# Kernel tuning notes

Measured on AMD Instinct MI355X. Metric: run time of the kernel, lower is better.

Reference implementation:

```python
import jax, jax.numpy as jnp
import numpy as np

LN_EPS = 1e-5

def setup_inputs() -> dict:
    key = jax.random.key(0)
    k1, k2, k3, k4 = jax.random.split(key, 4)
    B, N, F, O = 8, 2048, 256, 256
    x = jax.random.normal(k1, (B, N, F), dtype=jnp.float32)
    adj = jax.random.uniform(k2, (B, N, N), dtype=jnp.float32)
    # LayerNorm affine params
    gamma = jnp.ones((F,), jnp.float32)
    beta = jnp.zeros((F,), jnp.float32)
    # Linear weights stored as [in, out] (torch stores [out, in]; math identical)
    W_self = jax.random.normal(k3, (F, O), dtype=jnp.float32) * (1.0 / np.sqrt(F))
    W_neigh = jax.random.normal(k4, (F, O), dtype=jnp.float32) * (1.0 / np.sqrt(F))
    return {"x": x, "adj": adj, "gamma": gamma, "beta": beta,
            "W_self": W_self, "W_neigh": W_neigh}

def reference(x, adj, gamma, beta, W_self, W_neigh):
    # LayerNorm over last dim
    mu = jnp.mean(x, axis=-1, keepdims=True)
    var = jnp.mean(jnp.square(x - mu), axis=-1, keepdims=True)
    xn = (x - mu) * jax.lax.rsqrt(var + LN_EPS) * gamma + beta

    # Normalized Laplacian: I - D_out^{-1/2} A D_in^{-1/2}
    # out_degree = column sums (dim=1), in_degree = row sums (dim=2)
    d_out = jnp.sum(adj, axis=1)   # [B, N]
    d_in = jnp.sum(adj, axis=2)    # [B, N]
    s_out = jnp.where(d_out != 0, jax.lax.rsqrt(d_out), 0.0)
    s_in = jnp.where(d_in != 0, jax.lax.rsqrt(d_in), 0.0)
    # diag(s_out) @ A @ diag(s_in) == row/col elementwise rescale (no N^3 work)
    A_norm = s_out[:, :, None] * adj * s_in[:, None, :]
    eye = jnp.eye(adj.shape[1], dtype=adj.dtype)
    L = eye[None, :, :] - A_norm    # [B, N, N]

    neighbor = jnp.einsum('bij,bjf->bif', L, xn)   # [B, N, F]
    pre = xn @ W_self + neighbor @ W_neigh          # [B, N, O]
    return jax.nn.softplus(pre)
```

## Files before the change

### kernel.cpp

```cpp
#include <hip/hip_runtime.h>
#include <stdint.h>

#define B_ 8
#define N_ 2048
#define F_ 256

typedef unsigned short u16;
typedef __attribute__((ext_vector_type(8))) short bf16x8;
typedef __attribute__((ext_vector_type(4))) float f32x4;

__device__ __forceinline__ u16 f2bf(float f) {
    uint32_t u = __builtin_bit_cast(uint32_t, f);
    u += 0x7FFFu + ((u >> 16) & 1u);
    return (u16)(u >> 16);
}

__device__ __forceinline__ void gload_lds16(const void* g, void* lds_uniform_base) {
    __builtin_amdgcn_global_load_lds(
        (const __attribute__((address_space(1))) uint32_t*)g,
        (__attribute__((address_space(3))) uint32_t*)lds_uniform_base, 16, 0, 0);
}

__global__ __launch_bounds__(256) void k_deg(const float* __restrict__ adj,
                                             float* __restrict__ deg_row,
                                             float* __restrict__ pcol) {
    const int b = blockIdx.y, panel = blockIdx.x;
    const int t = threadIdx.x, w = t >> 6, l = t & 63;
    const float* base = adj + ((size_t)b * N_ + (size_t)panel * 32) * N_;
    float c0[4], c1[4];
#pragma unroll
    for (int e = 0; e < 4; ++e) { c0[e] = 0.f; c1[e] = 0.f; }
    __shared__ float rs[32][4];
#pragma unroll 4
    for (int r = 0; r < 32; ++r) {
        const float4 v0 = *(const float4*)(base + (size_t)r * N_ + t * 4);
        const float4 v1 = *(const float4*)(base + (size_t)r * N_ + 1024 + t * 4);
        c0[0] += v0.x; c0[1] += v0.y; c0[2] += v0.z; c0[3] += v0.w;
        c1[0] += v1.x; c1[1] += v1.y; c1[2] += v1.z; c1[3] += v1.w;
        float s = (v0.x + v0.y) + (v0.z + v0.w) + (v1.x + v1.y) + (v1.z + v1.w);
#pragma unroll
        for (int off = 32; off; off >>= 1) s += __shfl_xor(s, off);
        if (l == 0) rs[r][w] = s;
    }
    float4* pc = (float4*)(pcol + ((size_t)(b * 64 + panel)) * N_);
    pc[t]       = make_float4(c0[0], c0[1], c0[2], c0[3]);
    pc[t + 256] = make_float4(c1[0], c1[1], c1[2], c1[3]);
    __syncthreads();
    if (t < 32)
        deg_row[(size_t)b * N_ + panel * 32 + t] = rs[t][0] + rs[t][1] + rs[t][2] + rs[t][3];
}

__global__ __launch_bounds__(256) void k_dcol(const float* __restrict__ pcol,
                                              float* __restrict__ deg_col) {
    const int tid = blockIdx.x * 256 + threadIdx.x;
    const int b = tid >> 11, j = tid & 2047;
    const float* p = pcol + (size_t)b * 64 * N_ + j;
    float s = 0.f;
#pragma unroll
    for (int g = 0; g < 64; ++g) s += p[(size_t)g * N_];
    deg_col[tid] = s;
}

__global__ __launch_bounds__(256) void k_ln(const float* __restrict__ x,
                                            const float* __restrict__ gamma,
                                            const float* __restrict__ beta,
                                            const float* __restrict__ deg_row,
                                            u16* __restrict__ xn,
                                            u16* __restrict__ yT) {
    const int b = blockIdx.y, panel = blockIdx.x;
    const int t = threadIdx.x, w = t >> 6, l = t & 63;
    __shared__ u16 yt[256 * 34];
    float g[4], be[4];
#pragma unroll
    for (int m = 0; m < 4; ++m) { g[m] = gamma[l + 64 * m]; be[m] = beta[l + 64 * m]; }
    for (int rr = 0; rr < 8; ++rr) {
        const int jj = w * 8 + rr;
        const int j = panel * 32 + jj;
        const float* xp = x + ((size_t)b * N_ + j) * F_;
        float v[4], s = 0.f, ss = 0.f;
#pragma unroll
        for (int m = 0; m < 4; ++m) { v[m] = xp[l + 64 * m]; s += v[m]; ss += v[m] * v[m]; }
#pragma unroll
        for (int off = 32; off; off >>= 1) { s += __shfl_xor(s, off); ss += __shfl_xor(ss, off); }
        const float mu = s * (1.f / 256.f);
        const float var = ss * (1.f / 256.f) - mu * mu;
        const float rstd = rsqrtf(var + 1e-5f);
        const float d = deg_row[(size_t)b * N_ + j];
        const float sin_ = (d != 0.f) ? rsqrtf(d) : 0.f;
        u16* xnp = xn + ((size_t)b * N_ + j) * F_;
#pragma unroll
        for (int m = 0; m < 4; ++m) {
            const float xv = (v[m] - mu) * rstd * g[m] + be[m];
            xnp[l + 64 * m] = f2bf(xv);
            yt[(l + 64 * m) * 34 + jj] = f2bf(sin_ * xv);
        }
    }
    __syncthreads();
#pragma unroll
    for (int m2 = 0; m2 < 2; ++m2) {
        const int f = (t >> 1) + 128 * m2;
        const int jj0 = (t & 1) * 16;
        uint32_t vals[8];
#pragma unroll
        for (int e = 0; e < 8; ++e) vals[e] = *(const uint32_t*)&yt[f * 34 + jj0 + 2 * e];
        uint4* dst = (uint4*)(yT + ((size_t)b * F_ + f) * N_ + panel * 32 + jj0);
        dst[0] = make_uint4(vals[0], vals[1], vals[2], vals[3]);
        dst[1] = make_uint4(vals[4], vals[5], vals[6], vals[7]);
    }
}

__global__ __launch_bounds__(256) void k_wprep(const float* __restrict__ Ws,
                                               const float* __restrict__ Wn,
                                               u16* __restrict__ WcT,
                                               u16* __restrict__ WnT) {
    const int k = blockIdx.x, o = threadIdx.x;
    const float a = Ws[k * 256 + o], q = Wn[k * 256 + o];
    WcT[o * 256 + k] = f2bf(a + q);
    WnT[o * 256 + k] = f2bf(-q);
}

__global__ __launch_bounds__(512) void k_gemm1(const float* __restrict__ adj,
                                               const u16* __restrict__ yT,
                                               const float* __restrict__ deg_col,
                                               u16* __restrict__ z) {
    const int i = blockIdx.x;
    const int b = i & 7;
    const int kk = i >> 3;
    const int nt = kk & 1;
    const int m = kk >> 1;
    const int i0 = m * 128, f0 = nt * 128;
    const int t = threadIdx.x, w = t >> 6, l = t & 63;
    const int wr = w >> 2, wc = w & 3;
    alignas(16) __shared__ u16 As[128 * 32];
    alignas(16) __shared__ u16 Bs[128 * 32];
    f32x4 acc[4][2];
#pragma unroll
    for (int mi = 0; mi < 4; ++mi)
#pragma unroll
        for (int ni = 0; ni < 2; ++ni) acc[mi][ni] = (f32x4)0.f;

    const float* abase = adj + ((size_t)b * N_ + i0) * N_;
    const u16* ybase = yT + ((size_t)b * F_ + f0) * (size_t)N_;
    const int o = w * 1024 + l * 16;
    const int fr = o >> 6, jb = (o & 63) >> 1;

    for (int kt = 0; kt < 64; ++kt) {
        const int k0 = kt * 32;
        gload_lds16(ybase + (size_t)fr * N_ + k0 + jb, (char*)Bs + (w << 10));
#pragma unroll
        for (int q = 0; q < 2; ++q) {
            const int idx = t + 512 * q;
            const int row = idx >> 3, jq = idx & 7;
            const float4 v = *(const float4*)(abase + (size_t)row * N_ + k0 + jq * 4);
            const uint32_t u0 = (uint32_t)f2bf(v.x) | ((uint32_t)f2bf(v.y) << 16);
            const uint32_t u1 = (uint32_t)f2bf(v.z) | ((uint32_t)f2bf(v.w) << 16);
            *(uint2*)&As[row * 32 + jq * 4] = make_uint2(u0, u1);
        }
        __syncthreads();
        bf16x8 af[4], bfr[2];
#pragma unroll
        for (int mi = 0; mi < 4; ++mi)
            af[mi] = *(const bf16x8*)&As[(wr * 64 + mi * 16 + (l & 15)) * 32 + (l >> 4) * 8];
#pragma unroll
        for (int ni = 0; ni < 2; ++ni)
            bfr[ni] = *(const bf16x8*)&Bs[(wc * 32 + ni * 16 + (l & 15)) * 32 + (l >> 4) * 8];
#pragma unroll
        for (int mi = 0; mi < 4; ++mi)
#pragma unroll
            for (int ni = 0; ni < 2; ++ni)
                acc[mi][ni] = __builtin_amdgcn_mfma_f32_16x16x32_bf16(af[mi], bfr[ni], acc[mi][ni], 0, 0, 0);
        __syncthreads();
    }
#pragma unroll
    for (int mi = 0; mi < 4; ++mi) {
#pragma unroll
        for (int r = 0; r < 4; ++r) {
            const int row = i0 + wr * 64 + mi * 16 + (l >> 4) * 4 + r;
            const float d = deg_col[(size_t)b * N_ + row];
            const float so = (d != 0.f) ? rsqrtf(d) : 0.f;
#pragma unroll
            for (int ni = 0; ni < 2; ++ni) {
                const int col = f0 + wc * 32 + ni * 16 + (l & 15);
                z[((size_t)b * N_ + row) * F_ + col] = f2bf(so * acc[mi][ni][r]);
            }
        }
    }
}

__global__ __launch_bounds__(512) void k_gemm2(const u16* __restrict__ xn,
                                               const u16* __restrict__ z,
                                               const u16* __restrict__ WcT,
                                               const u16* __restrict__ WnT,
                                               float* __restrict__ out) {
    const int i = blockIdx.x;
    const int xcd = i & 7;
    const int kk = i >> 3;
    const int nt = kk & 1;
    const int mt = xcd + 8 * (kk >> 1);
    const int r0 = mt * 128, o0 = nt * 128;
    const int t = threadIdx.x, w = t >> 6, l = t & 63;
    const int wr = w >> 2, wc = w & 3;
    alignas(16) __shared__ u16 As[128 * 32];
    alignas(16) __shared__ u16 Bs[128 * 32];
    f32x4 acc[4][2];
#pragma unroll
    for (int mi = 0; mi < 4; ++mi)
#pragma unroll
        for (int ni = 0; ni < 2; ++ni) acc[mi][ni] = (f32x4)0.f;

    const int o = w * 1024 + l * 16;
    const int row = o >> 6, cb = (o & 63) >> 1;

    for (int kt = 0; kt < 16; ++kt) {
        const u16* asrc = (kt < 8) ? xn : z;
        const u16* bsrc = (kt < 8) ? WcT : WnT;
        const int kk0 = (kt & 7) * 32;
        gload_lds16(asrc + (size_t)(r0 + row) * F_ + kk0 + cb, (char*)As + (w << 10));
        gload_lds16(bsrc + (size_t)(o0 + row) * F_ + kk0 + cb, (char*)Bs + (w << 10));
        __syncthreads();
        bf16x8 af[4], bfr[2];
#pragma unroll
        for (int mi = 0; mi < 4; ++mi)
            af[mi] = *(const bf16x8*)&As[(wr * 64 + mi * 16 + (l & 15)) * 32 + (l >> 4) * 8];
#pragma unroll
        for (int ni = 0; ni < 2; ++ni)
            bfr[ni] = *(const bf16x8*)&Bs[(wc * 32 + ni * 16 + (l & 15)) * 32 + (l >> 4) * 8];
#pragma unroll
        for (int mi = 0; mi < 4; ++mi)
#pragma unroll
            for (int ni = 0; ni < 2; ++ni)
                acc[mi][ni] = __builtin_amdgcn_mfma_f32_16x16x32_bf16(af[mi], bfr[ni], acc[mi][ni], 0, 0, 0);
        __syncthreads();
    }
#pragma unroll
    for (int mi = 0; mi < 4; ++mi) {
#pragma unroll
        for (int r = 0; r < 4; ++r) {
            const int rr = r0 + wr * 64 + mi * 16 + (l >> 4) * 4 + r;
#pragma unroll
            for (int ni = 0; ni < 2; ++ni) {
                const int cc = o0 + wc * 32 + ni * 16 + (l & 15);
                const float p = acc[mi][ni][r];
                out[(size_t)rr * F_ + cc] = (p > 20.f) ? p : log1pf(expf(p));
            }
        }
    }
}

extern "C" void kernel_launch(void* const* d_in, const int* in_sizes, int n_in,
                              void* d_out, int out_size, void* d_ws, size_t ws_size,
                              hipStream_t stream) {
    (void)in_sizes; (void)n_in; (void)out_size; (void)ws_size;
    const float* x     = (const float*)d_in[0];
    const float* adj   = (const float*)d_in[1];
    const float* gamma = (const float*)d_in[2];
    const float* beta  = (const float*)d_in[3];
    const float* Ws    = (const float*)d_in[4];
    const float* Wn    = (const float*)d_in[5];
    float* out = (float*)d_out;

    char* ws = (char*)d_ws;
    float* deg_row = (float*)(ws + 0);
    float* deg_col = (float*)(ws + 65536);
    u16* xn  = (u16*)(ws + 131072);
    u16* yT  = (u16*)(ws + 131072 + 8388608);
    u16* z   = (u16*)(ws + 131072 + 2 * 8388608);
    u16* WcT = (u16*)(ws + 131072 + 3 * 8388608);
    u16* WnT = (u16*)(ws + 131072 + 3 * 8388608 + 131072);
    float* pcol = (float*)z;

    k_deg  <<<dim3(64, 8), 256, 0, stream>>>(adj, deg_row, pcol);
    k_dcol <<<64, 256, 0, stream>>>(pcol, deg_col);
    k_wprep<<<256, 256, 0, stream>>>(Ws, Wn, WcT, WnT);
    k_ln   <<<dim3(64, 8), 256, 0, stream>>>(x, gamma, beta, deg_row, xn, yT);
    k_gemm1<<<256, 512, 0, stream>>>(adj, yT, deg_col, z);
    k_gemm2<<<256, 512, 0, stream>>>(xn, z, WcT, WnT, out);
}
```

Baseline: 323.5 us.

## Fuse prep kernels, retile gemm1 to full-F tiles, double-buffer both GEMMs

Three small preparation kernels (column-degree reduce, LayerNorm/transpose, weight prep) are merged into one launch that branches on block index, removing two launch gaps. gemm1 now uses 64x256 tiles covering all of F, so each adjacency row block is read and converted once instead of twice. It also double-buffers LDS so the next tile's loads overlap the current MFMAs with a single barrier per step. gemm2 gets the same double buffering, at the cost of more LDS and some register pressure.

```diff
diff --git a/kernel.cpp b/kernel.cpp
--- a/kernel.cpp
+++ b/kernel.cpp
@@ -50,137 +50,154 @@
         deg_row[(size_t)b * N_ + panel * 32 + t] = rs[t][0] + rs[t][1] + rs[t][2] + rs[t][3];
 }
 
-__global__ __launch_bounds__(256) void k_dcol(const float* __restrict__ pcol,
-                                              float* __restrict__ deg_col) {
-    const int tid = blockIdx.x * 256 + threadIdx.x;
-    const int b = tid >> 11, j = tid & 2047;
-    const float* p = pcol + (size_t)b * 64 * N_ + j;
-    float s = 0.f;
-#pragma unroll
-    for (int g = 0; g < 64; ++g) s += p[(size_t)g * N_];
-    deg_col[tid] = s;
-}
-
-__global__ __launch_bounds__(256) void k_ln(const float* __restrict__ x,
-                                            const float* __restrict__ gamma,
-                                            const float* __restrict__ beta,
-                                            const float* __restrict__ deg_row,
-                                            u16* __restrict__ xn,
-                                            u16* __restrict__ yT) {
-    const int b = blockIdx.y, panel = blockIdx.x;
-    const int t = threadIdx.x, w = t >> 6, l = t & 63;
+__global__ __launch_bounds__(256) void k_mid(const float* __restrict__ x,
+                                             const float* __restrict__ gamma,
+                                             const float* __restrict__ beta,
+                                             const float* __restrict__ deg_row,
+                                             const float* __restrict__ pcol,
+                                             const float* __restrict__ Ws,
+                                             const float* __restrict__ Wn,
+                                             u16* __restrict__ xn,
+                                             u16* __restrict__ yT,
+                                             float* __restrict__ deg_col,
+                                             u16* __restrict__ WcT,
+                                             u16* __restrict__ WnT) {
+    const int bx = blockIdx.x;
+    const int t = threadIdx.x;
     __shared__ u16 yt[256 * 34];
-    float g[4], be[4];
-#pragma unroll
-    for (int m = 0; m < 4; ++m) { g[m] = gamma[l + 64 * m]; be[m] = beta[l + 64 * m]; }
-    for (int rr = 0; rr < 8; ++rr) {
-        const int jj = w * 8 + rr;
-        const int j = panel * 32 + jj;
-        const float* xp = x + ((size_t)b * N_ + j) * F_;
-        float v[4], s = 0.f, ss = 0.f;
-#pragma unroll
-        for (int m = 0; m < 4; ++m) { v[m] = xp[l + 64 * m]; s += v[m]; ss += v[m] * v[m]; }
-#pragma unroll
-        for (int off = 32; off; off >>= 1) { s += __shfl_xor(s, off); ss += __shfl_xor(ss, off); }
-        const float mu = s * (1.f / 256.f);
-        const float var = ss * (1.f / 256.f) - mu * mu;
-        const float rstd = rsqrtf(var + 1e-5f);
-        const float d = deg_row[(size_t)b * N_ + j];
-        const float sin_ = (d != 0.f) ? rsqrtf(d) : 0.f;
-        u16* xnp = xn + ((size_t)b * N_ + j) * F_;
-#pragma unroll
-        for (int m = 0; m < 4; ++m) {
-            const float xv = (v[m] - mu) * rstd * g[m] + be[m];
-            xnp[l + 64 * m] = f2bf(xv);
-            yt[(l + 64 * m) * 34 + jj] = f2bf(sin_ * xv);
-        }
-    }
-    __syncthreads();
-#pragma unroll
-    for (int m2 = 0; m2 < 2; ++m2) {
-        const int f = (t >> 1) + 128 * m2;
-        const int jj0 = (t & 1) * 16;
-        uint32_t vals[8];
-#pragma unroll
-        for (int e = 0; e < 8; ++e) vals[e] = *(const uint32_t*)&yt[f * 34 + jj0 + 2 * e];
-        uint4* dst = (uint4*)(yT + ((size_t)b * F_ + f) * N_ + panel * 32 + jj0);
-        dst[0] = make_uint4(vals[0], vals[1], vals[2], vals[3]);
-        dst[1] = make_uint4(vals[4], vals[5], vals[6], vals[7]);
-    }
-}
-
-__global__ __launch_bounds__(256) void k_wprep(const float* __restrict__ Ws,
-                                               const float* __restrict__ Wn,
-                                               u16* __restrict__ WcT,
-                                               u16* __restrict__ WnT) {
-    const int k = blockIdx.x, o = threadIdx.x;
-    const float a = Ws[k * 256 + o], q = Wn[k * 256 + o];
-    WcT[o * 256 + k] = f2bf(a + q);
-    WnT[o * 256 + k] = f2bf(-q);
+    if (bx < 512) {
+        const int b = bx >> 6, panel = bx & 63;
+        const int w = t >> 6, l = t & 63;
+        float g[4], be[4];
+#pragma unroll
+        for (int m = 0; m < 4; ++m) { g[m] = gamma[l + 64 * m]; be[m] = beta[l + 64 * m]; }
+        for (int rr = 0; rr < 8; ++rr) {
+            const int jj = w * 8 + rr;
+            const int j = panel * 32 + jj;
+            const float* xp = x + ((size_t)b * N_ + j) * F_;
+            float v[4], s = 0.f, ss = 0.f;
+#pragma unroll
+            for (int m = 0; m < 4; ++m) { v[m] = xp[l + 64 * m]; s += v[m]; ss += v[m] * v[m]; }
+#pragma unroll
+            for (int off = 32; off; off >>= 1) { s += __shfl_xor(s, off); ss += __shfl_xor(ss, off); }
+            const float mu = s * (1.f / 256.f);
+            const float var = ss * (1.f / 256.f) - mu * mu;
+            const float rstd = rsqrtf(var + 1e-5f);
+            const float d = deg_row[(size_t)b * N_ + j];
+            const float sin_ = (d != 0.f) ? rsqrtf(d) : 0.f;
+            u16* xnp = xn + ((size_t)b * N_ + j) * F_;
+#pragma unroll
+            for (int m = 0; m < 4; ++m) {
+                const float xv = (v[m] - mu) * rstd * g[m] + be[m];
+                xnp[l + 64 * m] = f2bf(xv);
+                yt[(l + 64 * m) * 34 + jj] = f2bf(sin_ * xv);
+            }
+        }
+        __syncthreads();
+#pragma unroll
+        for (int m2 = 0; m2 < 2; ++m2) {
+            const int f = (t >> 1) + 128 * m2;
+            const int jj0 = (t & 1) * 16;
+            uint32_t vals[8];
+#pragma unroll
+            for (int e = 0; e < 8; ++e) vals[e] = *(const uint32_t*)&yt[f * 34 + jj0 + 2 * e];
+            uint4* dst = (uint4*)(yT + ((size_t)b * F_ + f) * N_ + panel * 32 + jj0);
+            dst[0] = make_uint4(vals[0], vals[1], vals[2], vals[3]);
+            dst[1] = make_uint4(vals[4], vals[5], vals[6], vals[7]);
+        }
+    } else if (bx < 576) {
+        const int tid = (bx - 512) * 256 + t;
+        const int b = tid >> 11, j = tid & 2047;
+        const float* p = pcol + (size_t)b * 64 * N_ + j;
+        float s = 0.f;
+#pragma unroll
+        for (int g = 0; g < 64; ++g) s += p[(size_t)g * N_];
+        deg_col[tid] = s;
+    } else {
+        const int rel = bx - 576;
+#pragma unroll 4
+        for (int e = 0; e < 32; ++e) {
+            const int idx = rel * 8192 + e * 256 + t;
+            const int k = idx >> 8, o = idx & 255;
+            const float a = Ws[idx], q = Wn[idx];
+            WcT[o * 256 + k] = f2bf(a + q);
+            WnT[o * 256 + k] = f2bf(-q);
+        }
+    }
 }
 
 __global__ __launch_bounds__(512) void k_gemm1(const float* __restrict__ adj,
                                                const u16* __restrict__ yT,
                                                const float* __restrict__ deg_col,
                                                u16* __restrict__ z) {
-    const int i = blockIdx.x;
-    const int b = i & 7;
-    const int kk = i >> 3;
-    const int nt = kk & 1;
-    const int m = kk >> 1;
-    const int i0 = m * 128, f0 = nt * 128;
+    const int blk = blockIdx.x;
+    const int b = blk & 7;
+    const int m = blk >> 3;
+    const int i0 = m * 64;
     const int t = threadIdx.x, w = t >> 6, l = t & 63;
     const int wr = w >> 2, wc = w & 3;
-    alignas(16) __shared__ u16 As[128 * 32];
-    alignas(16) __shared__ u16 Bs[128 * 32];
-    f32x4 acc[4][2];
-#pragma unroll
-    for (int mi = 0; mi < 4; ++mi)
-#pragma unroll
-        for (int ni = 0; ni < 2; ++ni) acc[mi][ni] = (f32x4)0.f;
+    alignas(16) __shared__ u16 As[2][64 * 32];
+    alignas(16) __shared__ u16 Bs[2][256 * 32];
+    f32x4 acc[2][4];
+#pragma unroll
+    for (int mi = 0; mi < 2; ++mi)
+#pragma unroll
+        for (int ni = 0; ni < 4; ++ni) acc[mi][ni] = (f32x4)0.f;
 
     const float* abase = adj + ((size_t)b * N_ + i0) * N_;
-    const u16* ybase = yT + ((size_t)b * F_ + f0) * (size_t)N_;
+    const u16* ybase = yT + (size_t)b * F_ * (size_t)N_;
+    const int ar = t >> 3, aj = t & 7;
     const int o = w * 1024 + l * 16;
     const int fr = o >> 6, jb = (o & 63) >> 1;
 
+    {
+        const float4 av = *(const float4*)(abase + (size_t)ar * N_ + aj * 4);
+        gload_lds16(ybase + (size_t)fr * N_ + jb, (char*)&Bs[0][0] + (w << 10));
+        gload_lds16(ybase + (size_t)(fr + 128) * N_ + jb, (char*)&Bs[0][0] + 8192 + (w << 10));
+        const uint32_t u0 = (uint32_t)f2bf(av.x) | ((uint32_t)f2bf(av.y) << 16);
+        const uint32_t u1 = (uint32_t)f2bf(av.z) | ((uint32_t)f2bf(av.w) << 16);
+        *(uint2*)&As[0][ar * 32 + aj * 4] = make_uint2(u0, u1);
+    }
+    __syncthreads();
+
     for (int kt = 0; kt < 64; ++kt) {
-        const int k0 = kt * 32;
-        gload_lds16(ybase + (size_t)fr * N_ + k0 + jb, (char*)Bs + (w << 10));
-#pragma unroll
-        for (int q = 0; q < 2; ++q) {
-            const int idx = t + 512 * q;
-            const int row = idx >> 3, jq = idx & 7;
-            const float4 v = *(const float4*)(abase + (size_t)row * N_ + k0 + jq * 4);
-            const uint32_t u0 = (uint32_t)f2bf(v.x) | ((uint32_t)f2bf(v.y) << 16);
-            const uint32_t u1 = (uint32_t)f2bf(v.z) | ((uint32_t)f2bf(v.w) << 16);
-            *(uint2*)&As[row * 32 + jq * 4] = make_uint2(u0, u1);
+        const int cb = kt & 1, nb = cb ^ 1;
+        float4 an;
+        if (kt < 63) {
+            const int k0 = (kt + 1) * 32;
+            an = *(const float4*)(abase + (size_t)ar * N_ + k0 + aj * 4);
+            gload_lds16(ybase + (size_t)fr * N_ + k0 + jb, (char*)&Bs[nb][0] + (w << 10));
+            gload_lds16(ybase + (size_t)(fr + 128) * N_ + k0 + jb, (char*)&Bs[nb][0] + 8192 + (w << 10));
+        }
+        bf16x8 af[2], bfr[4];
+#pragma unroll
+        for (int mi = 0; mi < 2; ++mi)
+            af[mi] = *(const bf16x8*)&As[cb][(wr * 32 + mi * 16 + (l & 15)) * 32 + (l >> 4) * 8];
+#pragma unroll
+        for (int ni = 0; ni < 4; ++ni)
+            bfr[ni] = *(const bf16x8*)&Bs[cb][(wc * 64 + ni * 16 + (l & 15)) * 32 + (l >> 4) * 8];
+#pragma unroll
+        for (int mi = 0; mi < 2; ++mi)
+#pragma unroll
+            for (int ni = 0; ni < 4; ++ni)
+                acc[mi][ni] = __builtin_amdgcn_mfma_f32_16x16x32_bf16(af[mi], bfr[ni], acc[mi][ni], 0, 0, 0);
+        if (kt < 63) {
+            const uint32_t u0 = (uint32_t)f2bf(an.x) | ((uint32_t)f2bf(an.y) << 16);
+            const uint32_t u1 = (uint32_t)f2bf(an.z) | ((uint32_t)f2bf(an.w) << 16);
+            *(uint2*)&As[nb][ar * 32 + aj * 4] = make_uint2(u0, u1);
         }
         __syncthreads();
-        bf16x8 af[4], bfr[2];
-#pragma unroll
-        for (int mi = 0; mi < 4; ++mi)
-            af[mi] = *(const bf16x8*)&As[(wr * 64 + mi * 16 + (l & 15)) * 32 + (l >> 4) * 8];
-#pragma unroll
-        for (int ni = 0; ni < 2; ++ni)
-            bfr[ni] = *(const bf16x8*)&Bs[(wc * 32 + ni * 16 + (l & 15)) * 32 + (l >> 4) * 8];
-#pragma unroll
-        for (int mi = 0; mi < 4; ++mi)
-#pragma unroll
-            for (int ni = 0; ni < 2; ++ni)
-                acc[mi][ni] = __builtin_amdgcn_mfma_f32_16x16x32_bf16(af[mi], bfr[ni], acc[mi][ni], 0, 0, 0);
-        __syncthreads();
-    }
-#pragma unroll
-    for (int mi = 0; mi < 4; ++mi) {
+    }
+#pragma unroll
+    for (int mi = 0; mi < 2; ++mi) {
 #pragma unroll
         for (int r = 0; r < 4; ++r) {
-            const int row = i0 + wr * 64 + mi * 16 + (l >> 4) * 4 + r;
+            const int row = i0 + wr * 32 + mi * 16 + (l >> 4) * 4 + r;
             const float d = deg_col[(size_t)b * N_ + row];
             const float so = (d != 0.f) ? rsqrtf(d) : 0.f;
 #pragma unroll
-            for (int ni = 0; ni < 2; ++ni) {
-                const int col = f0 + wc * 32 + ni * 16 + (l & 15);
+            for (int ni = 0; ni < 4; ++ni) {
+                const int col = wc * 64 + ni * 16 + (l & 15);
                 z[((size_t)b * N_ + row) * F_ + col] = f2bf(so * acc[mi][ni][r]);
             }
         }
@@ -200,8 +217,8 @@
     const int r0 = mt * 128, o0 = nt * 128;
     const int t = threadIdx.x, w = t >> 6, l = t & 63;
     const int wr = w >> 2, wc = w & 3;
-    alignas(16) __shared__ u16 As[128 * 32];
-    alignas(16) __shared__ u16 Bs[128 * 32];
+    alignas(16) __shared__ u16 As[2][128 * 32];
+    alignas(16) __shared__ u16 Bs[2][128 * 32];
     f32x4 acc[4][2];
 #pragma unroll
     for (int mi = 0; mi < 4; ++mi)
@@ -209,22 +226,29 @@
         for (int ni = 0; ni < 2; ++ni) acc[mi][ni] = (f32x4)0.f;
 
     const int o = w * 1024 + l * 16;
-    const int row = o >> 6, cb = (o & 63) >> 1;
+    const int row = o >> 6, cb2 = (o & 63) >> 1;
+
+    gload_lds16(xn + (size_t)(r0 + row) * F_ + cb2, (char*)&As[0][0] + (w << 10));
+    gload_lds16(WcT + (size_t)(o0 + row) * F_ + cb2, (char*)&Bs[0][0] + (w << 10));
+    __syncthreads();
 
     for (int kt = 0; kt < 16; ++kt) {
-        const u16* asrc = (kt < 8) ? xn : z;
-        const u16* bsrc = (kt < 8) ? WcT : WnT;
-        const int kk0 = (kt & 7) * 32;
-        gload_lds16(asrc + (size_t)(r0 + row) * F_ + kk0 + cb, (char*)As + (w << 10));
-        gload_lds16(bsrc + (size_t)(o0 + row) * F_ + kk0 + cb, (char*)Bs + (w << 10));
-        __syncthreads();
+        const int cb = kt & 1, nb = cb ^ 1;
+        if (kt < 15) {
+            const int kn = kt + 1;
+            const u16* asrc = (kn < 8) ? xn : z;
+            const u16* bsrc = (kn < 8) ? WcT : WnT;
+            const int kk0 = (kn & 7) * 32;
+            gload_lds16(asrc + (size_t)(r0 + row) * F_ + kk0 + cb2, (char*)&As[nb][0] + (w << 10));
+            gload_lds16(bsrc + (size_t)(o0 + row) * F_ + kk0 + cb2, (char*)&Bs[nb][0] + (w << 10));
+        }
         bf16x8 af[4], bfr[2];
 #pragma unroll
         for (int mi = 0; mi < 4; ++mi)
-            af[mi] = *(const bf16x8*)&As[(wr * 64 + mi * 16 + (l & 15)) * 32 + (l >> 4) * 8];
+            af[mi] = *(const bf16x8*)&As[cb][(wr * 64 + mi * 16 + (l & 15)) * 32 + (l >> 4) * 8];
 #pragma unroll
         for (int ni = 0; ni < 2; ++ni)
-            bfr[ni] = *(const bf16x8*)&Bs[(wc * 32 + ni * 16 + (l & 15)) * 32 + (l >> 4) * 8];
+            bfr[ni] = *(const bf16x8*)&Bs[cb][(wc * 32 + ni * 16 + (l & 15)) * 32 + (l >> 4) * 8];
 #pragma unroll
         for (int mi = 0; mi < 4; ++mi)
 #pragma unroll
@@ -270,9 +294,8 @@
     float* pcol = (float*)z;
 
     k_deg  <<<dim3(64, 8), 256, 0, stream>>>(adj, deg_row, pcol);
-    k_dcol <<<64, 256, 0, stream>>>(pcol, deg_col);
-    k_wprep<<<256, 256, 0, stream>>>(Ws, Wn, WcT, WnT);
-    k_ln   <<<dim3(64, 8), 256, 0, stream>>>(x, gamma, beta, deg_row, xn, yT);
+    k_mid  <<<584, 256, 0, stream>>>(x, gamma, beta, deg_row, pcol, Ws, Wn,
+                                     xn, yT, deg_col, WcT, WnT);
     k_gemm1<<<256, 512, 0, stream>>>(adj, yT, deg_col, z);
     k_gemm2<<<256, 512, 0, stream>>>(xn, z, WcT, WnT, out);
 }
```

New measurement: 322.6 us. About the same (-0.3%).
